# Kernel optimization log

Hardware: AMD Instinct MI355X
Metric: run time of the kernel (lower is better)

Reference implementation:

```python
import jax, jax.numpy as jnp
import numpy as np


def _apply_ring(x, angles):
    """Apply x @ R^T where R = G_0 @ G_1 @ ... @ G_{n-1} with ring planes
    (k, (k+1) % n). Equivalent to applying G_k^T to x for k = n-1 .. 0:
      x[:, k] <- c*x[:, k] - s*x[:, j]
      x[:, j] <- s*x[:, k] + c*x[:, j]
    x: [B, n], angles: [n].
    """
    n = angles.shape[0]

    def step(xT, k):
        a = angles[k]
        c, s = jnp.cos(a), jnp.sin(a)
        j = jnp.mod(k + 1, n)
        xi = xT[k]
        xj = xT[j]
        xT = xT.at[k].set(c * xi - s * xj)
        xT = xT.at[j].set(s * xi + c * xj)
        return xT, None

    ks = jnp.arange(n - 1, -1, -1)  # reverse order: R^T = G_{n-1}^T ... G_0^T
    xT, _ = jax.lax.scan(step, x.T, ks)  # carry is [n, B]
    return xT.T


def setup_inputs() -> dict:
    key = jax.random.key(0)
    k_x, k_e, k_d = jax.random.split(key, 3)
    B, n, num_blocks = 8192, 1024, 4
    return {
        "x": jax.random.normal(k_x, (B, n), dtype=jnp.float32),
        "angles_enc": jax.random.normal(k_e, (num_blocks, n), dtype=jnp.float32),
        "angles_dec": jax.random.normal(k_d, (num_blocks, n), dtype=jnp.float32),
        "hidden_weight": jnp.zeros((1,), dtype=jnp.float32),
        "hidden_state": jnp.zeros((n,), dtype=jnp.float32),
    }


def reference(x, angles_enc, angles_dec, hidden_weight, hidden_state):
    num_blocks = angles_enc.shape[0]
    b = x
    for blk in range(num_blocks):
        b = _apply_ring(b, angles_enc[blk])
    # recurrent blend; weight uses the detached hidden_weight (original uses
    # numpy on .detach()), so stop_gradient matches the original semantics.
    w = jax.nn.sigmoid(jax.lax.stop_gradient(hidden_weight[0]))
    bottleneck = (1.0 - w) * b + w * hidden_state[None, :]
    out = bottleneck
    for blk in range(num_blocks):
        out = _apply_ring(out, angles_dec[blk])
    return (bottleneck, out)
```

## Files before the change

### kernel.cpp

```cpp
#include <hip/hip_runtime.h>
#include <math.h>

#define N_COLS 1024
#define NRINGS 8

#define TPR    64
#define CHUNK  16
#define PAIRS_PER_BLOCK 4

#define F_OFF    16384
#define A_OFF    24576
#define AUX_OFF  25088
#define WS_FLOATS 25104

__global__ __launch_bounds__(256)
void ced_setup(const float* __restrict__ ae,
               const float* __restrict__ ad,
               float* __restrict__ ws)
{
    __shared__ float2 ls[256];
    const int r   = blockIdx.x >> 2;
    const int b   = blockIdx.x & 3;
    const int tid = threadIdx.x;
    const int k   = (b << 8) + tid;
    const float* ang = (r < 4) ? (ae + (r << 10)) : (ad + ((r - 4) << 10));

    float sv, cv;
    sincosf(ang[k], &sv, &cv);
    if (k == N_COLS - 1) {
        ((float2*)(ws + AUX_OFF))[r] = make_float2(cv, sv);
        cv = 0.f; sv = -1.f;
    }
    ls[tid] = make_float2(cv, sv);
    __syncthreads();

    if (!(tid & 1)) {
        float2 e0 = ls[tid], e1 = ls[tid + 1];
        int t  = k >> 4;
        int jp = (k & 15) >> 1;
        ((float4*)ws)[(r*8 + jp)*64 + t] = make_float4(e0.x, e0.y, e1.x, e1.y);
    }

    if (tid < 64) {
        const int lt = tid >> 2;
        const int q  = tid & 3;
        const int t  = (b << 4) + lt;
        const int j0 = lt * CHUNK + 4 * q;
        float2 e0 = ls[j0], e1 = ls[j0+1], e2 = ls[j0+2], e3 = ls[j0+3];

        float f3 = e3.x;       float P = -e3.y;
        float f2 = e2.x * P;   P *= -e2.y;
        float f1 = e1.x * P;   P *= -e1.y;
        float f0 = e0.x * P;   P *= -e0.y;

        float ip = P;
        #pragma unroll
        for (int d = 1; d < 4; d <<= 1) {
            float tmp = __shfl_down(ip, d);
            if (q + d < 4) ip *= tmp;
        }
        float ex = __shfl_down(ip, 1);
        if (q == 3) ex = 1.f;
        f0 *= ex; f1 *= ex; f2 *= ex; f3 *= ex;

        ((float4*)(ws + F_OFF))[(r*4 + q)*64 + t] = make_float4(f0, f1, f2, f3);
        if (q == 0) ws[A_OFF + r*TPR + t] = ip;
    }
}

__global__ __launch_bounds__(256, 4)
void ced_main(const float* __restrict__ x,
              const float* __restrict__ ws,
              const float* __restrict__ hw,
              const float* __restrict__ hs,
              float* __restrict__ out, int B)
{
    const int tid = threadIdx.x;
    const int t   = tid & 63;
    const int pairRow = blockIdx.x * PAIRS_PER_BLOCK + (tid >> 6);
    const size_t rowA = (size_t)(2 * pairRow) * N_COLS;
    const size_t rowB = rowA + N_COLS;

    const float4* CSg  = (const float4*)ws;
    const float4* Fg   = (const float4*)(ws + F_OFF);
    const float*  Ag   = ws + A_OFF;
    const float2* AUXg = (const float2*)(ws + AUX_OFF);

    float ya[CHUNK], yb[CHUNK];
    {
        const float4* xa = (const float4*)(x + rowA + t * CHUNK);
        const float4* xb = (const float4*)(x + rowB + t * CHUNK);
        #pragma unroll
        for (int i = 0; i < 4; ++i) {
            float4 va = xa[i], vb = xb[i];
            ya[4*i] = va.x; ya[4*i+1] = va.y; ya[4*i+2] = va.z; ya[4*i+3] = va.w;
            yb[4*i] = vb.x; yb[4*i+1] = vb.y; yb[4*i+2] = vb.z; yb[4*i+3] = vb.w;
        }
    }

    const float w   = 1.f / (1.f + expf(-hw[0]));
    const float omw = 1.f - w;

    #pragma unroll 1
    for (int r = 0; r < NRINGS; ++r) {
        if (r == 4) {
            float4* oa = (float4*)(out + rowA + t * CHUNK);
            float4* ob = (float4*)(out + rowB + t * CHUNK);
            const float4* hp = (const float4*)(hs + t * CHUNK);
            #pragma unroll
            for (int i = 0; i < 4; ++i) {
                float4 h = hp[i];
                float4 na, nb2;
                na.x  = fmaf(omw, ya[4*i+0], w * h.x);
                na.y  = fmaf(omw, ya[4*i+1], w * h.y);
                na.z  = fmaf(omw, ya[4*i+2], w * h.z);
                na.w  = fmaf(omw, ya[4*i+3], w * h.w);
                nb2.x = fmaf(omw, yb[4*i+0], w * h.x);
                nb2.y = fmaf(omw, yb[4*i+1], w * h.y);
                nb2.z = fmaf(omw, yb[4*i+2], w * h.z);
                nb2.w = fmaf(omw, yb[4*i+3], w * h.w);
                oa[i] = na; ob[i] = nb2;
                ya[4*i+0] = na.x;  ya[4*i+1] = na.y;  ya[4*i+2] = na.z;  ya[4*i+3] = na.w;
                yb[4*i+0] = nb2.x; yb[4*i+1] = nb2.y; yb[4*i+2] = nb2.z; yb[4*i+3] = nb2.w;
            }
        }

        const float4* cs = CSg + r * 512;
        const float4* fp = Fg  + r * 256;
        const float2  cN  = AUXg[r];
        const float   saI = Ag[r * TPR + t];

        float y0a = __shfl(ya[0],       0);
        float yNa = __shfl(ya[CHUNK-1], 63);
        float y0b = __shfl(yb[0],       0);
        float yNb = __shfl(yb[CHUNK-1], 63);
        float CinitA = cN.x * yNa - cN.y * y0a;
        float CinitB = cN.x * yNb - cN.y * y0b;
        float x0nA   = fmaf(cN.y, yNa, cN.x * y0a);
        float x0nB   = fmaf(cN.y, yNb, cN.x * y0b);
        if (t == 0) { ya[0] = x0nA; yb[0] = x0nB; }

        float carA = 0.f, carB = 0.f, ztA = 0.f, ztB = 0.f;
        #pragma unroll
        for (int jp = CHUNK/2 - 1; jp >= 0; --jp) {
            float4 cs4 = cs[jp * 64 + t];
            const int j1 = 2*jp + 1;
            float z1a = fmaf(cs4.w, ya[j1], cs4.z * carA);
            float z1b = fmaf(cs4.w, yb[j1], cs4.z * carB);
            carA = fmaf(-cs4.w, carA, cs4.z * ya[j1]);
            carB = fmaf(-cs4.w, carB, cs4.z * yb[j1]);
            if (j1 == CHUNK - 1) { ztA = z1a; ztB = z1b; }
            else                 { ya[j1+1] = z1a; yb[j1+1] = z1b; }
            const int j0 = 2*jp;
            float z0a = fmaf(cs4.y, ya[j0], cs4.x * carA);
            float z0b = fmaf(cs4.y, yb[j0], cs4.x * carB);
            carA = fmaf(-cs4.y, carA, cs4.x * ya[j0]);
            carB = fmaf(-cs4.y, carB, cs4.x * yb[j0]);
            ya[j0+1] = z0a; yb[j0+1] = z0b;
        }

        float sa = saI, sbA = carA, sbB = carB;
        #pragma unroll
        for (int d = 1; d < TPR; d <<= 1) {
            float a2  = __shfl_down(sa,  d);
            float b2a = __shfl_down(sbA, d);
            float b2b = __shfl_down(sbB, d);
            if (t + d < TPR) {
                sbA = fmaf(sa, b2a, sbA);
                sbB = fmaf(sa, b2b, sbB);
                sa *= a2;
            }
        }
        float ea  = __shfl_down(sa,  1);
        float ebA = __shfl_down(sbA, 1);
        float ebB = __shfl_down(sbB, 1);
        float zfA = fmaf(sa, CinitA, sbA);
        float zfB = fmaf(sa, CinitB, sbB);
        float CinA = (t == TPR - 1) ? CinitA : fmaf(ea, CinitA, ebA);
        float CinB = (t == TPR - 1) ? CinitB : fmaf(ea, CinitB, ebB);

        #pragma unroll
        for (int qi = CHUNK/4 - 1; qi >= 0; --qi) {
            float4 f4 = fp[qi * 64 + t];
            const int j = 4*qi;
            if (j + 3 == CHUNK - 1) { ztA = fmaf(f4.w, CinA, ztA);
                                      ztB = fmaf(f4.w, CinB, ztB); }
            else                    { ya[j+4] = fmaf(f4.w, CinA, ya[j+4]);
                                      yb[j+4] = fmaf(f4.w, CinB, yb[j+4]); }
            ya[j+3] = fmaf(f4.z, CinA, ya[j+3]);  yb[j+3] = fmaf(f4.z, CinB, yb[j+3]);
            ya[j+2] = fmaf(f4.y, CinA, ya[j+2]);  yb[j+2] = fmaf(f4.y, CinB, yb[j+2]);
            ya[j+1] = fmaf(f4.x, CinA, ya[j+1]);  yb[j+1] = fmaf(f4.x, CinB, yb[j+1]);
        }

        float upA = __shfl_up(ztA, 1);
        float upB = __shfl_up(ztB, 1);
        ya[0] = (t == 0) ? zfA : upA;
        yb[0] = (t == 0) ? zfB : upB;
    }

    float4* oa = (float4*)(out + (size_t)B * N_COLS + rowA + t * CHUNK);
    float4* ob = (float4*)(out + (size_t)B * N_COLS + rowB + t * CHUNK);
    #pragma unroll
    for (int i = 0; i < 4; ++i) {
        oa[i] = make_float4(ya[4*i], ya[4*i+1], ya[4*i+2], ya[4*i+3]);
        ob[i] = make_float4(yb[4*i], yb[4*i+1], yb[4*i+2], yb[4*i+3]);
    }
}

__global__ __launch_bounds__(256, 2)
void ced_fallback(const float* __restrict__ x,
                  const float* __restrict__ ae,
                  const float* __restrict__ ad,
                  const float* __restrict__ hw,
                  const float* __restrict__ hs,
                  float* __restrict__ out, int B)
{
    __shared__ float2 s_cs[NRINGS * 64 * 16];
    __shared__ float  s_A [NRINGS * 16];
    __shared__ float2 s_aux[NRINGS];

    const int tid = threadIdx.x;
    for (int i = 0; i < 32; ++i) {
        int idx = i * 256 + tid;
        int r   = idx >> 10;
        int k   = idx & 1023;
        const float* ang = (r < 4) ? (ae + (r << 10)) : (ad + ((r - 4) << 10));
        float sv, cv;
        sincosf(ang[k], &sv, &cv);
        int t = k >> 6, j = k & 63;
        float2 e = make_float2(cv, sv);
        if (k == 1023) { s_aux[r] = e; e = make_float2(0.f, -1.f); }
        s_cs[(r * 64 + j) * 16 + t] = e;
    }
    __syncthreads();
    if (tid < NRINGS * 16) {
        int r = tid >> 4, t = tid & 15;
        float p = 1.f;
        for (int j = 0; j < 64; ++j) p *= -s_cs[(r * 64 + j) * 16 + t].y;
        s_A[tid] = p;
    }
    __syncthreads();

    const int lane      = tid & 63;
    const int g         = lane >> 4;
    const int t         = lane & 15;
    const int groupBase = lane & 48;
    const int row       = blockIdx.x * 16 + (tid >> 6) * 4 + g;

    const float* xr = x + (size_t)row * N_COLS + t * 64;
    float y[64];
    #pragma unroll
    for (int i = 0; i < 16; ++i) {
        float4 v = ((const float4*)xr)[i];
        y[4*i] = v.x; y[4*i+1] = v.y; y[4*i+2] = v.z; y[4*i+3] = v.w;
    }
    const float w   = 1.f / (1.f + expf(-hw[0]));
    const float omw = 1.f - w;

    for (int r = 0; r < NRINGS; ++r) {
        if (r == 4) {
            float4* ob = (float4*)(out + (size_t)row * N_COLS + t * 64);
            const float4* hp = (const float4*)(hs + t * 64);
            #pragma unroll
            for (int i = 0; i < 16; ++i) {
                float4 h = hp[i];
                float4 bn;
                bn.x = fmaf(omw, y[4*i+0], w * h.x);
                bn.y = fmaf(omw, y[4*i+1], w * h.y);
                bn.z = fmaf(omw, y[4*i+2], w * h.z);
                bn.w = fmaf(omw, y[4*i+3], w * h.w);
                ob[i] = bn;
                y[4*i+0] = bn.x; y[4*i+1] = bn.y; y[4*i+2] = bn.z; y[4*i+3] = bn.w;
            }
        }
        const float2* csr = s_cs + r * 64 * 16;
        const float2  cN  = s_aux[r];
        float y0 = __shfl(y[0],  groupBase);
        float yN = __shfl(y[63], groupBase + 15);
        float Cinit = cN.x * yN - cN.y * y0;
        float x0n   = fmaf(cN.y, yN, cN.x * y0);
        if (t == 0) y[0] = x0n;

        float carry = 0.f, ztmp = 0.f;
        #pragma unroll
        for (int j = 63; j >= 0; --j) {
            float2 cs = csr[j * 16 + t];
            float z   = fmaf(cs.y, y[j], cs.x * carry);
            carry     = fmaf(-cs.y, carry, cs.x * y[j]);
            if (j == 63) ztmp = z; else y[j + 1] = z;
        }
        float sa = s_A[r * 16 + t], sb = carry;
        #pragma unroll
        for (int d = 1; d < 16; d <<= 1) {
            float a2 = __shfl_down(sa, d);
            float b2 = __shfl_down(sb, d);
            if (t + d < 16) { sb = fmaf(sa, b2, sb); sa *= a2; }
        }
        float ea = __shfl_down(sa, 1);
        float eb = __shfl_down(sb, 1);
        float z0  = fmaf(sa, Cinit, sb);
        float Cin = (t == 15) ? Cinit : fmaf(ea, Cinit, eb);

        float P = 1.f;
        #pragma unroll
        for (int j = 63; j >= 0; --j) {
            float2 cs = csr[j * 16 + t];
            float f = cs.x * P;
            P = -cs.y * P;
            if (j == 63) ztmp = fmaf(f, Cin, ztmp);
            else         y[j + 1] = fmaf(f, Cin, y[j + 1]);
        }
        float up = __shfl_up(ztmp, 1);
        y[0] = (t == 0) ? z0 : up;
    }

    float4* oo = (float4*)(out + (size_t)B * N_COLS + (size_t)row * N_COLS + t * 64);
    #pragma unroll
    for (int i = 0; i < 16; ++i)
        oo[i] = make_float4(y[4*i], y[4*i+1], y[4*i+2], y[4*i+3]);
}

extern "C" void kernel_launch(void* const* d_in, const int* in_sizes, int n_in,
                              void* d_out, int out_size, void* d_ws, size_t ws_size,
                              hipStream_t stream) {
    const float* x  = (const float*)d_in[0];
    const float* ae = (const float*)d_in[1];
    const float* ad = (const float*)d_in[2];
    const float* hw = (const float*)d_in[3];
    const float* hs = (const float*)d_in[4];
    float* out = (float*)d_out;
    const int B = in_sizes[0] / N_COLS;

    if (ws_size >= WS_FLOATS * sizeof(float) && (B % (2 * PAIRS_PER_BLOCK)) == 0) {
        hipLaunchKernelGGL(ced_setup, dim3(32), dim3(256), 0, stream,
                           ae, ad, (float*)d_ws);
        hipLaunchKernelGGL(ced_main, dim3(B / (2 * PAIRS_PER_BLOCK)), dim3(256), 0, stream,
                           x, (const float*)d_ws, hw, hs, out, B);
    } else {
        hipLaunchKernelGGL(ced_fallback, dim3(B / 16), dim3(256), 0, stream,
                           x, ae, ad, hw, hs, out, B);
    }
}
```

Measured before the change: 123.9 us.

## Process four rows per wavefront and double-buffer ring coefficients in registers

Each wavefront now handles four rows instead of two, so every coefficient load and shuffle-scan step is shared across more independent rows. The per-ring rotation and correction coefficients are prefetched one ring ahead into a double-buffered register array, and the ring loop is fully unrolled. Launch bounds drop to two blocks per CU, trading occupancy and grid size (half as many blocks) for more register-resident work per thread and more instruction-level parallelism.

```diff
diff --git a/kernel.cpp b/kernel.cpp
--- a/kernel.cpp
+++ b/kernel.cpp
@@ -6,7 +6,7 @@
 
 #define TPR    64
 #define CHUNK  16
-#define PAIRS_PER_BLOCK 4
+#define QUADS_PER_BLOCK 4
 
 #define F_OFF    16384
 #define A_OFF    24576
@@ -68,49 +68,79 @@
     }
 }
 
-__global__ __launch_bounds__(256, 4)
+__global__ __launch_bounds__(256, 2)
 void ced_main(const float* __restrict__ x,
               const float* __restrict__ ws,
               const float* __restrict__ hw,
               const float* __restrict__ hs,
               float* __restrict__ out, int B)
 {
-    const int tid = threadIdx.x;
-    const int t   = tid & 63;
-    const int pairRow = blockIdx.x * PAIRS_PER_BLOCK + (tid >> 6);
-    const size_t rowA = (size_t)(2 * pairRow) * N_COLS;
+    const int tid  = threadIdx.x;
+    const int t    = tid & 63;
+    const int quad = blockIdx.x * QUADS_PER_BLOCK + (tid >> 6);
+    const size_t rowA = (size_t)(4 * quad) * N_COLS;
     const size_t rowB = rowA + N_COLS;
+    const size_t rowC = rowB + N_COLS;
+    const size_t rowD = rowC + N_COLS;
 
     const float4* CSg  = (const float4*)ws;
     const float4* Fg   = (const float4*)(ws + F_OFF);
     const float*  Ag   = ws + A_OFF;
     const float2* AUXg = (const float2*)(ws + AUX_OFF);
 
-    float ya[CHUNK], yb[CHUNK];
+    float4 csR[2][8];
+    float4 fvR[2][4];
+    #pragma unroll
+    for (int jp = 0; jp < 8; ++jp) csR[0][jp] = CSg[jp * 64 + t];
+    #pragma unroll
+    for (int qi = 0; qi < 4; ++qi) fvR[0][qi] = Fg[qi * 64 + t];
+
+    float ya[CHUNK], yb[CHUNK], yc[CHUNK], yd[CHUNK];
     {
         const float4* xa = (const float4*)(x + rowA + t * CHUNK);
         const float4* xb = (const float4*)(x + rowB + t * CHUNK);
+        const float4* xc = (const float4*)(x + rowC + t * CHUNK);
+        const float4* xd = (const float4*)(x + rowD + t * CHUNK);
         #pragma unroll
         for (int i = 0; i < 4; ++i) {
-            float4 va = xa[i], vb = xb[i];
+            float4 va = xa[i], vb = xb[i], vc = xc[i], vd = xd[i];
             ya[4*i] = va.x; ya[4*i+1] = va.y; ya[4*i+2] = va.z; ya[4*i+3] = va.w;
             yb[4*i] = vb.x; yb[4*i+1] = vb.y; yb[4*i+2] = vb.z; yb[4*i+3] = vb.w;
+            yc[4*i] = vc.x; yc[4*i+1] = vc.y; yc[4*i+2] = vc.z; yc[4*i+3] = vc.w;
+            yd[4*i] = vd.x; yd[4*i+1] = vd.y; yd[4*i+2] = vd.z; yd[4*i+3] = vd.w;
         }
     }
 
     const float w   = 1.f / (1.f + expf(-hw[0]));
     const float omw = 1.f - w;
 
-    #pragma unroll 1
+    #pragma unroll
     for (int r = 0; r < NRINGS; ++r) {
+        const int cb = r & 1;
+        const int nb = cb ^ 1;
+
+        if (r < NRINGS - 1) {
+            #pragma unroll
+            for (int jp = 0; jp < 8; ++jp)
+                csR[nb][jp] = CSg[(r + 1) * 512 + jp * 64 + t];
+            #pragma unroll
+            for (int qi = 0; qi < 4; ++qi)
+                fvR[nb][qi] = Fg[(r + 1) * 256 + qi * 64 + t];
+        }
+
+        const float  saI = Ag[r * TPR + t];
+        const float2 cN  = AUXg[r];
+
         if (r == 4) {
             float4* oa = (float4*)(out + rowA + t * CHUNK);
             float4* ob = (float4*)(out + rowB + t * CHUNK);
+            float4* oc = (float4*)(out + rowC + t * CHUNK);
+            float4* od = (float4*)(out + rowD + t * CHUNK);
             const float4* hp = (const float4*)(hs + t * CHUNK);
             #pragma unroll
             for (int i = 0; i < 4; ++i) {
                 float4 h = hp[i];
-                float4 na, nb2;
+                float4 na, nb2, nc, nd;
                 na.x  = fmaf(omw, ya[4*i+0], w * h.x);
                 na.y  = fmaf(omw, ya[4*i+1], w * h.y);
                 na.z  = fmaf(omw, ya[4*i+2], w * h.z);
@@ -119,91 +149,138 @@
                 nb2.y = fmaf(omw, yb[4*i+1], w * h.y);
                 nb2.z = fmaf(omw, yb[4*i+2], w * h.z);
                 nb2.w = fmaf(omw, yb[4*i+3], w * h.w);
-                oa[i] = na; ob[i] = nb2;
+                nc.x  = fmaf(omw, yc[4*i+0], w * h.x);
+                nc.y  = fmaf(omw, yc[4*i+1], w * h.y);
+                nc.z  = fmaf(omw, yc[4*i+2], w * h.z);
+                nc.w  = fmaf(omw, yc[4*i+3], w * h.w);
+                nd.x  = fmaf(omw, yd[4*i+0], w * h.x);
+                nd.y  = fmaf(omw, yd[4*i+1], w * h.y);
+                nd.z  = fmaf(omw, yd[4*i+2], w * h.z);
+                nd.w  = fmaf(omw, yd[4*i+3], w * h.w);
+                oa[i] = na; ob[i] = nb2; oc[i] = nc; od[i] = nd;
                 ya[4*i+0] = na.x;  ya[4*i+1] = na.y;  ya[4*i+2] = na.z;  ya[4*i+3] = na.w;
                 yb[4*i+0] = nb2.x; yb[4*i+1] = nb2.y; yb[4*i+2] = nb2.z; yb[4*i+3] = nb2.w;
+                yc[4*i+0] = nc.x;  yc[4*i+1] = nc.y;  yc[4*i+2] = nc.z;  yc[4*i+3] = nc.w;
+                yd[4*i+0] = nd.x;  yd[4*i+1] = nd.y;  yd[4*i+2] = nd.z;  yd[4*i+3] = nd.w;
             }
         }
-
-        const float4* cs = CSg + r * 512;
-        const float4* fp = Fg  + r * 256;
-        const float2  cN  = AUXg[r];
-        const float   saI = Ag[r * TPR + t];
 
         float y0a = __shfl(ya[0],       0);
         float yNa = __shfl(ya[CHUNK-1], 63);
         float y0b = __shfl(yb[0],       0);
         float yNb = __shfl(yb[CHUNK-1], 63);
+        float y0c = __shfl(yc[0],       0);
+        float yNc = __shfl(yc[CHUNK-1], 63);
+        float y0d = __shfl(yd[0],       0);
+        float yNd = __shfl(yd[CHUNK-1], 63);
         float CinitA = cN.x * yNa - cN.y * y0a;
         float CinitB = cN.x * yNb - cN.y * y0b;
+        float CinitC = cN.x * yNc - cN.y * y0c;
+        float CinitD = cN.x * yNd - cN.y * y0d;
         float x0nA   = fmaf(cN.y, yNa, cN.x * y0a);
         float x0nB   = fmaf(cN.y, yNb, cN.x * y0b);
-        if (t == 0) { ya[0] = x0nA; yb[0] = x0nB; }
-
-        float carA = 0.f, carB = 0.f, ztA = 0.f, ztB = 0.f;
+        float x0nC   = fmaf(cN.y, yNc, cN.x * y0c);
+        float x0nD   = fmaf(cN.y, yNd, cN.x * y0d);
+        if (t == 0) { ya[0] = x0nA; yb[0] = x0nB; yc[0] = x0nC; yd[0] = x0nD; }
+
+        float carA = 0.f, carB = 0.f, carC = 0.f, carD = 0.f;
+        float ztA = 0.f, ztB = 0.f, ztC = 0.f, ztD = 0.f;
         #pragma unroll
         for (int jp = CHUNK/2 - 1; jp >= 0; --jp) {
-            float4 cs4 = cs[jp * 64 + t];
+            float4 cs4 = csR[cb][jp];
             const int j1 = 2*jp + 1;
             float z1a = fmaf(cs4.w, ya[j1], cs4.z * carA);
             float z1b = fmaf(cs4.w, yb[j1], cs4.z * carB);
+            float z1c = fmaf(cs4.w, yc[j1], cs4.z * carC);
+            float z1d = fmaf(cs4.w, yd[j1], cs4.z * carD);
             carA = fmaf(-cs4.w, carA, cs4.z * ya[j1]);
             carB = fmaf(-cs4.w, carB, cs4.z * yb[j1]);
-            if (j1 == CHUNK - 1) { ztA = z1a; ztB = z1b; }
-            else                 { ya[j1+1] = z1a; yb[j1+1] = z1b; }
+            carC = fmaf(-cs4.w, carC, cs4.z * yc[j1]);
+            carD = fmaf(-cs4.w, carD, cs4.z * yd[j1]);
+            if (j1 == CHUNK - 1) { ztA = z1a; ztB = z1b; ztC = z1c; ztD = z1d; }
+            else                 { ya[j1+1] = z1a; yb[j1+1] = z1b;
+                                   yc[j1+1] = z1c; yd[j1+1] = z1d; }
             const int j0 = 2*jp;
             float z0a = fmaf(cs4.y, ya[j0], cs4.x * carA);
             float z0b = fmaf(cs4.y, yb[j0], cs4.x * carB);
+            float z0c = fmaf(cs4.y, yc[j0], cs4.x * carC);
+            float z0d = fmaf(cs4.y, yd[j0], cs4.x * carD);
             carA = fmaf(-cs4.y, carA, cs4.x * ya[j0]);
             carB = fmaf(-cs4.y, carB, cs4.x * yb[j0]);
-            ya[j0+1] = z0a; yb[j0+1] = z0b;
-        }
-
-        float sa = saI, sbA = carA, sbB = carB;
+            carC = fmaf(-cs4.y, carC, cs4.x * yc[j0]);
+            carD = fmaf(-cs4.y, carD, cs4.x * yd[j0]);
+            ya[j0+1] = z0a; yb[j0+1] = z0b; yc[j0+1] = z0c; yd[j0+1] = z0d;
+        }
+
+        float sa = saI, sbA = carA, sbB = carB, sbC = carC, sbD = carD;
         #pragma unroll
         for (int d = 1; d < TPR; d <<= 1) {
             float a2  = __shfl_down(sa,  d);
             float b2a = __shfl_down(sbA, d);
             float b2b = __shfl_down(sbB, d);
+            float b2c = __shfl_down(sbC, d);
+            float b2d = __shfl_down(sbD, d);
             if (t + d < TPR) {
                 sbA = fmaf(sa, b2a, sbA);
                 sbB = fmaf(sa, b2b, sbB);
+                sbC = fmaf(sa, b2c, sbC);
+                sbD = fmaf(sa, b2d, sbD);
                 sa *= a2;
             }
         }
         float ea  = __shfl_down(sa,  1);
         float ebA = __shfl_down(sbA, 1);
         float ebB = __shfl_down(sbB, 1);
+        float ebC = __shfl_down(sbC, 1);
+        float ebD = __shfl_down(sbD, 1);
         float zfA = fmaf(sa, CinitA, sbA);
         float zfB = fmaf(sa, CinitB, sbB);
+        float zfC = fmaf(sa, CinitC, sbC);
+        float zfD = fmaf(sa, CinitD, sbD);
         float CinA = (t == TPR - 1) ? CinitA : fmaf(ea, CinitA, ebA);
         float CinB = (t == TPR - 1) ? CinitB : fmaf(ea, CinitB, ebB);
+        float CinC = (t == TPR - 1) ? CinitC : fmaf(ea, CinitC, ebC);
+        float CinD = (t == TPR - 1) ? CinitD : fmaf(ea, CinitD, ebD);
 
         #pragma unroll
         for (int qi = CHUNK/4 - 1; qi >= 0; --qi) {
-            float4 f4 = fp[qi * 64 + t];
+            float4 f4 = fvR[cb][qi];
             const int j = 4*qi;
-            if (j + 3 == CHUNK - 1) { ztA = fmaf(f4.w, CinA, ztA);
-                                      ztB = fmaf(f4.w, CinB, ztB); }
-            else                    { ya[j+4] = fmaf(f4.w, CinA, ya[j+4]);
-                                      yb[j+4] = fmaf(f4.w, CinB, yb[j+4]); }
+            if (j + 3 == CHUNK - 1) {
+                ztA = fmaf(f4.w, CinA, ztA); ztB = fmaf(f4.w, CinB, ztB);
+                ztC = fmaf(f4.w, CinC, ztC); ztD = fmaf(f4.w, CinD, ztD);
+            } else {
+                ya[j+4] = fmaf(f4.w, CinA, ya[j+4]); yb[j+4] = fmaf(f4.w, CinB, yb[j+4]);
+                yc[j+4] = fmaf(f4.w, CinC, yc[j+4]); yd[j+4] = fmaf(f4.w, CinD, yd[j+4]);
+            }
             ya[j+3] = fmaf(f4.z, CinA, ya[j+3]);  yb[j+3] = fmaf(f4.z, CinB, yb[j+3]);
+            yc[j+3] = fmaf(f4.z, CinC, yc[j+3]);  yd[j+3] = fmaf(f4.z, CinD, yd[j+3]);
             ya[j+2] = fmaf(f4.y, CinA, ya[j+2]);  yb[j+2] = fmaf(f4.y, CinB, yb[j+2]);
+            yc[j+2] = fmaf(f4.y, CinC, yc[j+2]);  yd[j+2] = fmaf(f4.y, CinD, yd[j+2]);
             ya[j+1] = fmaf(f4.x, CinA, ya[j+1]);  yb[j+1] = fmaf(f4.x, CinB, yb[j+1]);
+            yc[j+1] = fmaf(f4.x, CinC, yc[j+1]);  yd[j+1] = fmaf(f4.x, CinD, yd[j+1]);
         }
 
         float upA = __shfl_up(ztA, 1);
         float upB = __shfl_up(ztB, 1);
+        float upC = __shfl_up(ztC, 1);
+        float upD = __shfl_up(ztD, 1);
         ya[0] = (t == 0) ? zfA : upA;
         yb[0] = (t == 0) ? zfB : upB;
+        yc[0] = (t == 0) ? zfC : upC;
+        yd[0] = (t == 0) ? zfD : upD;
     }
 
     float4* oa = (float4*)(out + (size_t)B * N_COLS + rowA + t * CHUNK);
     float4* ob = (float4*)(out + (size_t)B * N_COLS + rowB + t * CHUNK);
+    float4* oc = (float4*)(out + (size_t)B * N_COLS + rowC + t * CHUNK);
+    float4* od = (float4*)(out + (size_t)B * N_COLS + rowD + t * CHUNK);
     #pragma unroll
     for (int i = 0; i < 4; ++i) {
         oa[i] = make_float4(ya[4*i], ya[4*i+1], ya[4*i+2], ya[4*i+3]);
         ob[i] = make_float4(yb[4*i], yb[4*i+1], yb[4*i+2], yb[4*i+3]);
+        oc[i] = make_float4(yc[4*i], yc[4*i+1], yc[4*i+2], yc[4*i+3]);
+        od[i] = make_float4(yd[4*i], yd[4*i+1], yd[4*i+2], yd[4*i+3]);
     }
 }
 
@@ -331,10 +408,10 @@
     float* out = (float*)d_out;
     const int B = in_sizes[0] / N_COLS;
 
-    if (ws_size >= WS_FLOATS * sizeof(float) && (B % (2 * PAIRS_PER_BLOCK)) == 0) {
+    if (ws_size >= WS_FLOATS * sizeof(float) && (B % (4 * QUADS_PER_BLOCK)) == 0) {
         hipLaunchKernelGGL(ced_setup, dim3(32), dim3(256), 0, stream,
                            ae, ad, (float*)d_ws);
-        hipLaunchKernelGGL(ced_main, dim3(B / (2 * PAIRS_PER_BLOCK)), dim3(256), 0, stream,
+        hipLaunchKernelGGL(ced_main, dim3(B / (4 * QUADS_PER_BLOCK)), dim3(256), 0, stream,
                            x, (const float*)d_ws, hw, hs, out, B);
     } else {
         hipLaunchKernelGGL(ced_fallback, dim3(B / 16), dim3(256), 0, stream,
```

Measured after the change: 144.2 us. 1.16x slower.
